# Kernel tuning notes

Hardware: AMD Instinct MI355X
Metric: run time of the kernel (lower is better)

The kernel has to match this reference:

```python
import jax, jax.numpy as jnp
import numpy as np

B, S, D = 2, 2048, 2048
NQ, NKV, H = 16, 8, 256
G = NQ // NKV
SOFT_CAP = 50.0
WINDOW = 1024
MAX_WAVELENGTH = 10000.0


def _rope(x, start_index=0):
    # keras_hub RotaryEmbedding (rotate-half) followed by Gemma's interleave
    # reshape: stack(split(x,2,-1),axis=-1).reshape(shape). Net effect:
    # out[..., 2i] = x1*cos - x2*sin, out[..., 2i+1] = x2*cos + x1*sin.
    b, s, n, h = x.shape
    half = h // 2
    inv_freq = 1.0 / (MAX_WAVELENGTH ** (jnp.arange(0, h, 2, dtype=jnp.float32) / h))
    positions = start_index + jnp.arange(s, dtype=jnp.float32)
    freq = positions[:, None] * inv_freq[None, :]            # (s, h/2)
    cos = jnp.cos(freq)[None, :, None, :].astype(x.dtype)     # (1,s,1,h/2)
    sin = jnp.sin(freq)[None, :, None, :].astype(x.dtype)
    x1, x2 = x[..., :half], x[..., half:]
    r1 = x1 * cos - x2 * sin
    r2 = x2 * cos + x1 * sin
    return jnp.stack([r1, r2], axis=-1).reshape(b, s, n, h)


def setup_inputs() -> dict:
    key = jax.random.key(0)
    ks = jax.random.split(key, 5)
    x = jax.random.normal(ks[0], (B, S, D), dtype=jnp.float32)
    Wq = jax.random.normal(ks[1], (NQ, D, H), dtype=jnp.float32) * 0.02
    Wk = jax.random.normal(ks[2], (NKV, D, H), dtype=jnp.float32) * 0.02
    Wv = jax.random.normal(ks[3], (NKV, D, H), dtype=jnp.float32) * 0.02
    Wo = jax.random.normal(ks[4], (NQ, H, D), dtype=jnp.float32) * 0.02
    attention_mask = jnp.tril(jnp.ones((S, S), dtype=jnp.float32))  # causal
    return {"x": x, "Wq": Wq, "Wk": Wk, "Wv": Wv, "Wo": Wo,
            "attention_mask": attention_mask}


def reference(x, Wq, Wk, Wv, Wo, attention_mask):
    q = _rope(jnp.einsum('btd,ndh->btnh', x, Wq))   # (B,S,NQ,H)
    k = _rope(jnp.einsum('bsd,kdh->bskh', x, Wk))   # (B,S,NKV,H)
    v = jnp.einsum('bsd,kdh->bskh', x, Wv)          # (B,S,NKV,H)

    q = q * jnp.asarray(1.0 / np.sqrt(H), dtype=q.dtype)
    q = q.reshape(B, S, NKV, G, H)
    logits = jnp.einsum('btkgh,bskh->bkgts', q, k).astype(jnp.float32)

    # logit soft-cap
    logits = jnp.tanh(logits / SOFT_CAP) * SOFT_CAP

    # sliding-window band AND causal mask
    ones = jnp.ones((S, S), dtype=jnp.float32)
    sliding = jnp.triu(ones, -(WINDOW - 1)) * jnp.tril(ones, WINDOW - 1)
    mask = sliding * attention_mask                  # (S,S)

    # keras Softmax with mask: masked positions get -1e9 (fp32)
    masked = jnp.where(mask[None, None, None, :, :] > 0, logits,
                       jnp.float32(-1e9))
    probs = jax.nn.softmax(masked, axis=-1).astype(x.dtype)

    av = jnp.einsum('bkgts,bskh->btkgh', probs, v).reshape(B, S, NQ, H)

    # zero rows with no attended tokens (original causal mask)
    na = jnp.all(attention_mask == 0, axis=-1, keepdims=True)[..., None]  # (S,1,1)
    av = jnp.where(na, jnp.zeros_like(av), av)

    return jnp.einsum('btnh,nhd->btd', av, Wo)
```

## Files before the change

### kernel.cpp

```cpp
#include <hip/hip_runtime.h>
#include <stdint.h>

typedef __bf16 bf16_t;
typedef __bf16 bf16x8 __attribute__((ext_vector_type(8)));
typedef __bf16 bf16x4 __attribute__((ext_vector_type(4)));
typedef float f32x4 __attribute__((ext_vector_type(4)));

#define DEV static __device__ __forceinline__

#define SB 2
#define SS 2048
#define SD 2048
#define SNQ 16
#define SNKV 8
#define SH 256
#define SWIN 1024
#define QKVP 8192

DEV void async_ld16(const void* g, void* lds) {
  __builtin_amdgcn_global_load_lds(
      (const __attribute__((address_space(1))) void*)g,
      (__attribute__((address_space(3))) void*)lds, 16, 0, 0);
}

__global__ __launch_bounds__(256) void cvt_kernel(const float* __restrict__ in,
                                                  bf16_t* __restrict__ out) {
  int i = blockIdx.x * 256 + threadIdx.x;
  float4 v = ((const float4*)in)[i];
  bf16x4 o = {(bf16_t)v.x, (bf16_t)v.y, (bf16_t)v.z, (bf16_t)v.w};
  *(bf16x4*)(out + (size_t)i * 4) = o;
}

__global__ __launch_bounds__(256) void wtrans3_kernel(const float* __restrict__ Wq,
                                                      const float* __restrict__ Wk,
                                                      const float* __restrict__ Wv,
                                                      bf16_t* __restrict__ out) {
  __shared__ bf16_t T[64 * 72];
  const int zg = blockIdx.z;
  const float* ip = (zg < 16) ? (Wq + (size_t)zg * SD * SH)
                  : (zg < 24) ? (Wk + (size_t)(zg - 16) * SD * SH)
                              : (Wv + (size_t)(zg - 24) * SD * SH);
  bf16_t* op = out + (size_t)zg * SD * SH;
  const int r0 = blockIdx.y * 64, c0 = blockIdx.x * 64;
  const int tc = threadIdx.x & 15;
  const int tr = threadIdx.x >> 4;
#pragma unroll
  for (int i = 0; i < 4; ++i) {
    const int r = tr + i * 16;
    float4 v = *(const float4*)(ip + (size_t)(r0 + r) * SH + c0 + tc * 4);
    float vv[4] = {v.x, v.y, v.z, v.w};
#pragma unroll
    for (int e = 0; e < 4; ++e) {
      const int row = tc * 4 + e;
      *(bf16_t*)((char*)T + row * 144 + ((r * 2) ^ (((row >> 3) & 7) << 4))) =
          (bf16_t)vv[e];
    }
  }
  __syncthreads();
  const int tc2 = threadIdx.x & 7, tr2 = threadIdx.x >> 3;
#pragma unroll
  for (int i = 0; i < 2; ++i) {
    const int row = tr2 + i * 32;
    bf16x8 v = *(const bf16x8*)((const char*)T + row * 144 +
                                ((tc2 * 16) ^ (((row >> 3) & 7) << 4)));
    *(bf16x8*)(op + (size_t)(c0 + row) * SD + r0 + tc2 * 8) = v;
  }
}

__global__ __launch_bounds__(256) void wtrans_kernel(const float* __restrict__ in,
                                                     bf16_t* __restrict__ out,
                                                     int R, int C) {
  __shared__ bf16_t T[64 * 72];
  const float* ip = in;
  bf16_t* op = out;
  const int r0 = blockIdx.y * 64, c0 = blockIdx.x * 64;
  const int tc = threadIdx.x & 15;
  const int tr = threadIdx.x >> 4;
#pragma unroll
  for (int i = 0; i < 4; ++i) {
    const int r = tr + i * 16;
    float4 v = *(const float4*)(ip + (size_t)(r0 + r) * C + c0 + tc * 4);
    float vv[4] = {v.x, v.y, v.z, v.w};
#pragma unroll
    for (int e = 0; e < 4; ++e) {
      const int row = tc * 4 + e;
      *(bf16_t*)((char*)T + row * 144 + ((r * 2) ^ (((row >> 3) & 7) << 4))) =
          (bf16_t)vv[e];
    }
  }
  __syncthreads();
  const int tc2 = threadIdx.x & 7, tr2 = threadIdx.x >> 3;
#pragma unroll
  for (int i = 0; i < 2; ++i) {
    const int row = tr2 + i * 32;
    bf16x8 v = *(const bf16x8*)((const char*)T + row * 144 +
                                ((tc2 * 16) ^ (((row >> 3) & 7) << 4)));
    *(bf16x8*)(op + (size_t)(c0 + row) * R + r0 + tc2 * 8) = v;
  }
}

template <int BN, int MODE>
__global__ __launch_bounds__(512, 1) void gemm8p(const bf16_t* __restrict__ A,
                                                 const bf16_t* __restrict__ Bt,
                                                 void* __restrict__ Cout,
                                                 bf16_t* __restrict__ kbp,
                                                 bf16_t* __restrict__ vtp,
                                                 int M, int N, int K) {
  constexpr int WM = (BN == 256) ? 2 : 4;
  constexpr int WN = 8 / WM;
  constexpr int MQ = 4 / WM;
  constexpr int BH = BN / 128;
  constexpr int SMEM = 65536 + BH * 32768;
  __shared__ char smem[SMEM];
  bf16_t* AsBase = (bf16_t*)smem;
  bf16_t* BsBase = (bf16_t*)(smem + 65536);

  const int tid = threadIdx.x, lane = tid & 63, wid = tid >> 6;
  const int xcd = blockIdx.x & 7, ii = blockIdx.x >> 3;
  int by, bx;
  if (BN == 256) { by = (xcd & 1) * 8 + (ii >> 3); bx = (xcd >> 1) * 8 + (ii & 7); }
  else           { by = (xcd & 3) * 4 + (ii >> 3); bx = (xcd >> 2) * 8 + (ii & 7); }
  const int row0 = by << 8, col0 = bx * BN;
  const int wr = wid / WN, wc = wid % WN;
  const int lr = lane & 15, hi = lane >> 4;

  const bf16_t* Arow = A + (size_t)row0 * K;
  const bf16_t* Brow = Bt + (size_t)col0 * K;

  auto stageHA = [&](int t, int h) {
#pragma unroll
    for (int i = 0; i < 2; ++i) {
      const int f = tid + (i << 9);
      const int r = (h << 7) + (f >> 3), pc = f & 7;
      async_ld16(Arow + (size_t)r * K + (t << 6) + (pc ^ (r & 7)) * 8,
                 (char*)(AsBase + (t & 1) * (256 * 64)) + (h << 14) + f * 16);
    }
  };
  auto stageHB = [&](int t, int h) {
#pragma unroll
    for (int i = 0; i < 2; ++i) {
      const int f = tid + (i << 9);
      const int r = (h << 7) + (f >> 3), pc = f & 7;
      async_ld16(Brow + (size_t)r * K + (t << 6) + (pc ^ (r & 7)) * 8,
                 (char*)(BsBase + (t & 1) * (BN * 64)) + (h << 14) + f * 16);
    }
  };

  f32x4 acc[4 * MQ][4];
#pragma unroll
  for (int m = 0; m < 4 * MQ; ++m)
#pragma unroll
    for (int n = 0; n < 4; ++n) acc[m][n] = f32x4{0.f, 0.f, 0.f, 0.f};

  const int NT = K >> 6;
  stageHB(0, 0);
  if (BH == 2) stageHB(0, 1);
  stageHA(0, 0); stageHA(0, 1);
  asm volatile("s_waitcnt vmcnt(2)" ::: "memory");
  __builtin_amdgcn_s_barrier();
  __builtin_amdgcn_sched_barrier(0);

  for (int t = 0; t < NT; ++t) {
    const bool pre = (t + 1 < NT);
    const char* Ab = (const char*)(AsBase + (t & 1) * (256 * 64));
    const char* Bb = (const char*)(BsBase + (t & 1) * (BN * 64));
    bf16x8 bfr[4][2];

#pragma unroll
    for (int q = 0; q < 4; ++q) {
      if (q == 0) {
#pragma unroll
        for (int nf = 0; nf < 4; ++nf)
#pragma unroll
          for (int ks = 0; ks < 2; ++ks) {
            const int r = nf * (16 * WN) + wc * 16 + lr;
            bfr[nf][ks] = *(const bf16x8*)(Bb + r * 128 +
                                           ((((ks << 2) + hi) ^ (r & 7)) << 4));
          }
      }
      bf16x8 af[MQ][2];
#pragma unroll
      for (int mq = 0; mq < MQ; ++mq)
#pragma unroll
        for (int ks = 0; ks < 2; ++ks) {
          const int r = q * 64 + mq * (16 * WM) + wr * 16 + lr;
          af[mq][ks] = *(const bf16x8*)(Ab + r * 128 +
                                        ((((ks << 2) + hi) ^ (r & 7)) << 4));
        }
      if (pre) {
        if (BH == 2) {
          if (q == 0) stageHB(t + 1, 0);
          if (q == 1) stageHB(t + 1, 1);
          if (q == 2) stageHA(t + 1, 0);
          if (q == 3) stageHA(t + 1, 1);
        } else {
          if (q == 0) stageHB(t + 1, 0);
          if (q == 1) stageHA(t + 1, 0);
          if (q == 2) stageHA(t + 1, 1);
        }
      }
      __builtin_amdgcn_s_setprio(1);
#pragma unroll
      for (int mq = 0; mq < MQ; ++mq)
#pragma unroll
        for (int nf = 0; nf < 4; ++nf)
#pragma unroll
          for (int ks = 0; ks < 2; ++ks)
            acc[q * MQ + mq][nf] = __builtin_amdgcn_mfma_f32_16x16x32_bf16(
                af[mq][ks], bfr[nf][ks], acc[q * MQ + mq][nf], 0, 0, 0);
      __builtin_amdgcn_s_setprio(0);
      if (q == 1) {
        if (pre) asm volatile("s_waitcnt vmcnt(4)" ::: "memory");
        else     asm volatile("s_waitcnt vmcnt(0)" ::: "memory");
        __builtin_amdgcn_s_barrier();
        __builtin_amdgcn_sched_barrier(0);
      }
      if (q == 3 && pre) {
        asm volatile("s_waitcnt vmcnt(2)" ::: "memory");
        __builtin_amdgcn_s_barrier();
        __builtin_amdgcn_sched_barrier(0);
      }
    }
  }

  if (MODE == 1 && bx >= 16 && bx < 24) {
    const int kv = bx - 16;
#pragma unroll
    for (int mf = 0; mf < 4 * MQ; ++mf) {
      const int r = row0 + (mf / MQ) * 64 + (mf % MQ) * (16 * WM) + wr * 16 + hi * 4;
#pragma unroll
      for (int nfp = 0; nfp < 2; ++nfp) {
        const int h = nfp * 64 + wc * 16 + lr;
        const float inv = __expf((float)h * -0.07195578f);
#pragma unroll
        for (int j = 0; j < 4; ++j) {
          const int rg = r + j;
          const int tpos = rg & (SS - 1), b = rg >> 11;
          const float fr = (float)tpos * inv;
          const float cs = __cosf(fr), sn = __sinf(fr);
          const float x1 = acc[mf][nfp][j], x2 = acc[mf][nfp + 2][j];
          bf16_t* kp = kbp + ((size_t)(b * SNKV + kv) * SS + tpos) * SH + h;
          kp[0] = (bf16_t)(x1 * cs - x2 * sn);
          kp[128] = (bf16_t)(x2 * cs + x1 * sn);
        }
      }
    }
  } else if (MODE == 1 && bx >= 24) {
    bf16_t* T = (bf16_t*)smem;
    __syncthreads();
    const int kv = bx - 24;
#pragma unroll
    for (int mf = 0; mf < 4 * MQ; ++mf) {
      const int tl = (mf / MQ) * 64 + (mf % MQ) * (16 * WM) + wr * 16 + hi * 4;
#pragma unroll
      for (int nf = 0; nf < 4; ++nf) {
        const int h = nf * (16 * WN) + wc * 16 + lr;
        bf16x4 v4 = {(bf16_t)acc[mf][nf][0], (bf16_t)acc[mf][nf][1],
                     (bf16_t)acc[mf][nf][2], (bf16_t)acc[mf][nf][3]};
        *(bf16x4*)((char*)T + h * 512 + ((tl * 2) ^ ((h & 7) << 4))) = v4;
      }
    }
    __syncthreads();
    const int b = row0 >> 11, t0b = row0 & (SS - 1);
    bf16_t* vbase = vtp + (size_t)(b * SNKV + kv) * SH * SS;
#pragma unroll
    for (int it = 0; it < 16; ++it) {
      const int f = tid + (it << 9);
      const int h = f >> 5, sl = f & 31;
      bf16x8 v = *(const bf16x8*)((const char*)T + h * 512 +
                                  ((sl << 4) ^ ((h & 7) << 4)));
      *(bf16x8*)(vbase + (size_t)h * SS + t0b + sl * 8) = v;
    }
  } else {
#pragma unroll
    for (int mf = 0; mf < 4 * MQ; ++mf) {
      const int r = row0 + (mf / MQ) * 64 + (mf % MQ) * (16 * WM) + wr * 16 + hi * 4;
#pragma unroll
      for (int nf = 0; nf < 4; ++nf) {
        const int c = col0 + nf * (16 * WN) + wc * 16 + lr;
#pragma unroll
        for (int j = 0; j < 4; ++j) {
          if (MODE == 2)
            ((float*)Cout)[(size_t)(r + j) * N + c] = acc[mf][nf][j];
          else
            ((bf16_t*)Cout)[(size_t)(r + j) * N + c] = (bf16_t)acc[mf][nf][j];
        }
      }
    }
  }
}

#define QB 128
#define KVB 64
#define PP 72

__global__ __launch_bounds__(512, 2) void attn_kernel(
    const bf16_t* __restrict__ Q,
    const bf16_t* __restrict__ Kt,
    const bf16_t* __restrict__ Vt,
    bf16_t* __restrict__ AV) {
  __shared__ bf16_t Ks[2][KVB * SH];
  __shared__ bf16_t Vs[2][SH * KVB];
  __shared__ bf16_t Ps[QB * PP];

  const int tid = threadIdx.x, lane = tid & 63, wid = tid >> 6;
  const int x = blockIdx.x & 7;
  const int y = blockIdx.x >> 3;
  const int qt = 15 - (y & 15);
  const int head = (x << 1) | ((y >> 4) & 1);
  const int b = y >> 5;
  const int kvh = x;
  const int t0 = qt << 7;
  const int trw = t0 + wid * 16;
  const int lr = lane & 15, hi = lane >> 4;
  const int lk = hi << 3;
  const int lq = hi;

  bf16x8 qf[8];
  {
    const bf16_t* qp = Q + ((size_t)(b * SS + trw + lr)) * QKVP + head * SH + lk;
#pragma unroll
    for (int ks = 0; ks < 8; ++ks) qf[ks] = *(const bf16x8*)(qp + ks * 32);
    const float tpos = (float)(trw + lr);
#pragma unroll
    for (int ks = 0; ks < 4; ++ks) {
      bf16x8 a = qf[ks], b2 = qf[ks + 4];
      bf16x8 ra, rb;
#pragma unroll
      for (int e = 0; e < 8; ++e) {
        float c_ = (float)(ks * 32 + lk + e);
        float inv = __expf(c_ * -0.07195578f);
        float fr = tpos * inv;
        float cs = __cosf(fr), sn = __sinf(fr);
        float x1 = (float)a[e], x2 = (float)b2[e];
        ra[e] = (bf16_t)((x1 * cs - x2 * sn) * 0.0625f);
        rb[e] = (bf16_t)((x2 * cs + x1 * sn) * 0.0625f);
      }
      qf[ks] = ra; qf[ks + 4] = rb;
    }
  }

  f32x4 o[16];
#pragma unroll
  for (int i = 0; i < 16; ++i) o[i] = f32x4{0.f, 0.f, 0.f, 0.f};
  float lsum[4] = {0.f, 0.f, 0.f, 0.f};

  const bf16_t* Kb = Kt + (size_t)(b * SNKV + kvh) * SS * SH;
  const bf16_t* Vb = Vt + (size_t)(b * SNKV + kvh) * SH * SS;

  const int sv0 = (t0 >= SWIN) ? ((t0 >> 6) - 16) : 0;
  const int sv1 = (t0 >> 6) + 1;

  auto stage = [&](int s0, int d) {
#pragma unroll
    for (int it = 0; it < 4; ++it) {
      const int f = tid + (it << 9);
      {
        const int r = f >> 5, pc = f & 31;
        const int sc = pc ^ (r & 7);
        async_ld16(Kb + (size_t)(s0 + r) * SH + sc * 8, (char*)Ks[d] + f * 16);
      }
      {
        const int r = f >> 3, pc = f & 7;
        const int sc = pc ^ (r & 7);
        async_ld16(Vb + (size_t)r * SS + s0 + sc * 8, (char*)Vs[d] + f * 16);
      }
    }
  };

  stage(sv0 << 6, 0);
  __syncthreads();

  int cur = 0;
  for (int sv = sv0; sv <= sv1; ++sv, cur ^= 1) {
    if (sv < sv1) stage((sv + 1) << 6, cur ^ 1);

    const int s0 = sv << 6;
    const bool skip = (s0 > trw + 15) || (s0 + 63 < trw - (SWIN - 1));
    if (!skip) {
      const bf16_t* Kc = Ks[cur];
      const bf16_t* Vc = Vs[cur];
      f32x4 sacc[4];
#pragma unroll
      for (int nt = 0; nt < 4; ++nt) sacc[nt] = f32x4{0.f, 0.f, 0.f, 0.f};
      __builtin_amdgcn_s_setprio(1);
#pragma unroll
      for (int ks = 0; ks < 8; ++ks) {
#pragma unroll
        for (int nt = 0; nt < 4; ++nt) {
          const int R = nt * 16 + lr;
          bf16x8 kf = *(const bf16x8*)((const char*)Kc + R * 512 +
                                       (((ks * 4 + hi) ^ (R & 7)) << 4));
          sacc[nt] = __builtin_amdgcn_mfma_f32_16x16x32_bf16(qf[ks], kf, sacc[nt], 0, 0, 0);
        }
      }
      __builtin_amdgcn_s_setprio(0);

      const bool full = (s0 + 63 <= trw) && (s0 >= trw + 15 - (SWIN - 1));
      if (full) {
#pragma unroll
        for (int nt = 0; nt < 4; ++nt) {
#pragma unroll
          for (int j = 0; j < 4; ++j) {
            float u = sacc[nt][j] * 0.04f;
            float th = 50.f - 100.f * __builtin_amdgcn_rcpf(__expf(u) + 1.f);
            float p = __expf(th);
            lsum[j] += p;
            Ps[(wid * 16 + lq * 4 + j) * PP + nt * 16 + lr] = (bf16_t)p;
          }
        }
      } else {
#pragma unroll
        for (int nt = 0; nt < 4; ++nt) {
          const int s_ = s0 + nt * 16 + lr;
#pragma unroll
          for (int j = 0; j < 4; ++j) {
            const int t_ = trw + lq * 4 + j;
            float u = sacc[nt][j] * 0.04f;
            float th = 50.f - 100.f * __builtin_amdgcn_rcpf(__expf(u) + 1.f);
            const bool valid = (s_ <= t_) && (t_ - s_ < SWIN);
            float p = valid ? __expf(th) : 0.f;
            lsum[j] += p;
            Ps[(wid * 16 + lq * 4 + j) * PP + nt * 16 + lr] = (bf16_t)p;
          }
        }
      }

      __builtin_amdgcn_s_setprio(1);
#pragma unroll
      for (int ks = 0; ks < 2; ++ks) {
        bf16x8 pf = *(const bf16x8*)&Ps[(wid * 16 + lr) * PP + ks * 32 + lk];
#pragma unroll
        for (int nt = 0; nt < 16; ++nt) {
          const int R = nt * 16 + lr;
          bf16x8 vf = *(const bf16x8*)((const char*)Vc + R * 128 +
                                       (((ks * 4 + hi) ^ (R & 7)) << 4));
          o[nt] = __builtin_amdgcn_mfma_f32_16x16x32_bf16(pf, vf, o[nt], 0, 0, 0);
        }
      }
      __builtin_amdgcn_s_setprio(0);
    }

    __syncthreads();
  }

#pragma unroll
  for (int j = 0; j < 4; ++j) {
    float l = lsum[j];
    l += __shfl_xor(l, 1);
    l += __shfl_xor(l, 2);
    l += __shfl_xor(l, 4);
    l += __shfl_xor(l, 8);
    const float inv = 1.f / l;
    const int t_ = trw + lq * 4 + j;
    bf16_t* op = AV + ((size_t)(b * SS + t_)) * (SNQ * SH) + head * SH;
#pragma unroll
    for (int nt = 0; nt < 16; ++nt) op[nt * 16 + lr] = (bf16_t)(o[nt][j] * inv);
  }
}

extern "C" void kernel_launch(void* const* d_in, const int* in_sizes, int n_in,
                              void* d_out, int out_size, void* d_ws, size_t ws_size,
                              hipStream_t stream) {
  const float* x = (const float*)d_in[0];
  const float* Wq = (const float*)d_in[1];
  const float* Wk = (const float*)d_in[2];
  const float* Wv = (const float*)d_in[3];
  const float* Wo = (const float*)d_in[4];
  float* out = (float*)d_out;

  char* ws = (char*)d_ws;
  size_t off = 0;
  auto alloc = [&](size_t elems) {
    bf16_t* p = (bf16_t*)(ws + off);
    off += ((elems * 2 + 255) & ~(size_t)255);
    return p;
  };
  const size_t MS = (size_t)SB * SS;
  bf16_t* xb     = alloc(MS * SD);
  bf16_t* wqkvT  = alloc((size_t)QKVP * SD);
  bf16_t* woT    = alloc((size_t)SD * SNQ * SH);
  bf16_t* qkv    = alloc(MS * QKVP);
  bf16_t* kb     = alloc(MS * SNKV * SH);
  bf16_t* vt     = alloc(MS * SNKV * SH);
  bf16_t* av     = alloc(MS * SNQ * SH);
  (void)ws_size;

  cvt_kernel<<<(MS * SD / 4) / 256, 256, 0, stream>>>(x, xb);
  wtrans3_kernel<<<dim3(SH / 64, SD / 64, 32), 256, 0, stream>>>(Wq, Wk, Wv, wqkvT);
  wtrans_kernel<<<dim3(SD / 64, (SNQ * SH) / 64, 1), 256, 0, stream>>>(Wo, woT, SNQ * SH, SD);

  gemm8p<256, 1><<<512, 512, 0, stream>>>(xb, wqkvT, qkv, kb, vt, 4096, QKVP, 2048);

  attn_kernel<<<512, 512, 0, stream>>>(qkv, kb, vt, av);

  gemm8p<128, 2><<<256, 512, 0, stream>>>(av, woT, out, nullptr, nullptr, 4096, 2048, 4096);
}
```

Measured before the change: 326.4 us.

## Merge prep kernels and restructure GEMM k-loop into 2x2 A/B sub-tiles

Merges the x conversion and the three weight-transpose kernels into one launch, indexing the work by a flattened block id, to cut launch overhead. Restructures the GEMM inner loop so that A fragments for two 64-row quarters are loaded together and B fragments are loaded in halves. The next-tile async loads and the vmcnt/barrier points are re-spread across the four sub-steps. This changes register pressure and the overlap of loads with MFMA work, and the hand-tuned waitcnt values must exactly match the count of outstanding loads.

```diff
diff --git a/kernel.cpp b/kernel.cpp
--- a/kernel.cpp
+++ b/kernel.cpp
@@ -23,57 +23,39 @@
       (__attribute__((address_space(3))) void*)lds, 16, 0, 0);
 }
 
-__global__ __launch_bounds__(256) void cvt_kernel(const float* __restrict__ in,
-                                                  bf16_t* __restrict__ out) {
-  int i = blockIdx.x * 256 + threadIdx.x;
-  float4 v = ((const float4*)in)[i];
-  bf16x4 o = {(bf16_t)v.x, (bf16_t)v.y, (bf16_t)v.z, (bf16_t)v.w};
-  *(bf16x4*)(out + (size_t)i * 4) = o;
-}
-
-__global__ __launch_bounds__(256) void wtrans3_kernel(const float* __restrict__ Wq,
-                                                      const float* __restrict__ Wk,
-                                                      const float* __restrict__ Wv,
-                                                      bf16_t* __restrict__ out) {
+__global__ __launch_bounds__(256) void prep_kernel(
+    const float* __restrict__ x, const float* __restrict__ Wq,
+    const float* __restrict__ Wk, const float* __restrict__ Wv,
+    const float* __restrict__ Wo, bf16_t* __restrict__ xb,
+    bf16_t* __restrict__ wqkvT, bf16_t* __restrict__ woT) {
   __shared__ bf16_t T[64 * 72];
-  const int zg = blockIdx.z;
-  const float* ip = (zg < 16) ? (Wq + (size_t)zg * SD * SH)
-                  : (zg < 24) ? (Wk + (size_t)(zg - 16) * SD * SH)
-                              : (Wv + (size_t)(zg - 24) * SD * SH);
-  bf16_t* op = out + (size_t)zg * SD * SH;
-  const int r0 = blockIdx.y * 64, c0 = blockIdx.x * 64;
-  const int tc = threadIdx.x & 15;
-  const int tr = threadIdx.x >> 4;
-#pragma unroll
-  for (int i = 0; i < 4; ++i) {
-    const int r = tr + i * 16;
-    float4 v = *(const float4*)(ip + (size_t)(r0 + r) * SH + c0 + tc * 4);
-    float vv[4] = {v.x, v.y, v.z, v.w};
-#pragma unroll
-    for (int e = 0; e < 4; ++e) {
-      const int row = tc * 4 + e;
-      *(bf16_t*)((char*)T + row * 144 + ((r * 2) ^ (((row >> 3) & 7) << 4))) =
-          (bf16_t)vv[e];
-    }
-  }
-  __syncthreads();
-  const int tc2 = threadIdx.x & 7, tr2 = threadIdx.x >> 3;
-#pragma unroll
-  for (int i = 0; i < 2; ++i) {
-    const int row = tr2 + i * 32;
-    bf16x8 v = *(const bf16x8*)((const char*)T + row * 144 +
-                                ((tc2 * 16) ^ (((row >> 3) & 7) << 4)));
-    *(bf16x8*)(op + (size_t)(c0 + row) * SD + r0 + tc2 * 8) = v;
-  }
-}
-
-__global__ __launch_bounds__(256) void wtrans_kernel(const float* __restrict__ in,
-                                                     bf16_t* __restrict__ out,
-                                                     int R, int C) {
-  __shared__ bf16_t T[64 * 72];
-  const float* ip = in;
-  bf16_t* op = out;
-  const int r0 = blockIdx.y * 64, c0 = blockIdx.x * 64;
+  int bid = blockIdx.x;
+  if (bid < 8192) {
+    const int i = bid * 256 + threadIdx.x;
+    float4 v = ((const float4*)x)[i];
+    bf16x4 o = {(bf16_t)v.x, (bf16_t)v.y, (bf16_t)v.z, (bf16_t)v.w};
+    *(bf16x4*)(xb + (size_t)i * 4) = o;
+    return;
+  }
+  bid -= 8192;
+  const float* ip;
+  bf16_t* op;
+  int R, C, r0, c0;
+  if (bid < 4096) {
+    const int zg = bid >> 7, rest = bid & 127;
+    r0 = (rest >> 2) * 64;
+    c0 = (rest & 3) * 64;
+    ip = (zg < 16) ? (Wq + (size_t)zg * SD * SH)
+       : (zg < 24) ? (Wk + (size_t)(zg - 16) * SD * SH)
+                   : (Wv + (size_t)(zg - 24) * SD * SH);
+    op = wqkvT + (size_t)zg * SD * SH;
+    R = SD; C = SH;
+  } else {
+    bid -= 4096;
+    r0 = (bid >> 5) * 64;
+    c0 = (bid & 31) * 64;
+    ip = Wo; op = woT; R = SNQ * SH; C = SD;
+  }
   const int tc = threadIdx.x & 15;
   const int tr = threadIdx.x >> 4;
 #pragma unroll
@@ -153,10 +135,13 @@
     for (int n = 0; n < 4; ++n) acc[m][n] = f32x4{0.f, 0.f, 0.f, 0.f};
 
   const int NT = K >> 6;
-  stageHB(0, 0);
-  if (BH == 2) stageHB(0, 1);
-  stageHA(0, 0); stageHA(0, 1);
-  asm volatile("s_waitcnt vmcnt(2)" ::: "memory");
+  if (BH == 2) {
+    stageHB(0, 0); stageHA(0, 0); stageHB(0, 1); stageHA(0, 1);
+    asm volatile("s_waitcnt vmcnt(4)" ::: "memory");
+  } else {
+    stageHB(0, 0); stageHA(0, 0); stageHA(0, 1);
+    asm volatile("s_waitcnt vmcnt(2)" ::: "memory");
+  }
   __builtin_amdgcn_s_barrier();
   __builtin_amdgcn_sched_barrier(0);
 
@@ -164,61 +149,70 @@
     const bool pre = (t + 1 < NT);
     const char* Ab = (const char*)(AsBase + (t & 1) * (256 * 64));
     const char* Bb = (const char*)(BsBase + (t & 1) * (BN * 64));
-    bf16x8 bfr[4][2];
-
-#pragma unroll
-    for (int q = 0; q < 4; ++q) {
-      if (q == 0) {
-#pragma unroll
-        for (int nf = 0; nf < 4; ++nf)
+
+#pragma unroll
+    for (int pa = 0; pa < 2; ++pa) {
+      bf16x8 af[2][MQ][2];
+#pragma unroll
+      for (int qq = 0; qq < 2; ++qq)
+#pragma unroll
+        for (int mq = 0; mq < MQ; ++mq)
 #pragma unroll
           for (int ks = 0; ks < 2; ++ks) {
-            const int r = nf * (16 * WN) + wc * 16 + lr;
-            bfr[nf][ks] = *(const bf16x8*)(Bb + r * 128 +
+            const int r = (pa * 2 + qq) * 64 + mq * (16 * WM) + wr * 16 + lr;
+            af[qq][mq][ks] = *(const bf16x8*)(Ab + r * 128 +
+                                              ((((ks << 2) + hi) ^ (r & 7)) << 4));
+          }
+#pragma unroll
+      for (int pb = 0; pb < 2; ++pb) {
+        bf16x8 bfr[2][2];
+#pragma unroll
+        for (int bn = 0; bn < 2; ++bn)
+#pragma unroll
+          for (int ks = 0; ks < 2; ++ks) {
+            const int r = (pb * 2 + bn) * (16 * WN) + wc * 16 + lr;
+            bfr[bn][ks] = *(const bf16x8*)(Bb + r * 128 +
                                            ((((ks << 2) + hi) ^ (r & 7)) << 4));
           }
-      }
-      bf16x8 af[MQ][2];
-#pragma unroll
-      for (int mq = 0; mq < MQ; ++mq)
-#pragma unroll
-        for (int ks = 0; ks < 2; ++ks) {
-          const int r = q * 64 + mq * (16 * WM) + wr * 16 + lr;
-          af[mq][ks] = *(const bf16x8*)(Ab + r * 128 +
-                                        ((((ks << 2) + hi) ^ (r & 7)) << 4));
-        }
-      if (pre) {
-        if (BH == 2) {
-          if (q == 0) stageHB(t + 1, 0);
-          if (q == 1) stageHB(t + 1, 1);
-          if (q == 2) stageHA(t + 1, 0);
-          if (q == 3) stageHA(t + 1, 1);
-        } else {
-          if (q == 0) stageHB(t + 1, 0);
-          if (q == 1) stageHA(t + 1, 0);
-          if (q == 2) stageHA(t + 1, 1);
-        }
-      }
-      __builtin_amdgcn_s_setprio(1);
-#pragma unroll
-      for (int mq = 0; mq < MQ; ++mq)
-#pragma unroll
-        for (int nf = 0; nf < 4; ++nf)
-#pragma unroll
-          for (int ks = 0; ks < 2; ++ks)
-            acc[q * MQ + mq][nf] = __builtin_amdgcn_mfma_f32_16x16x32_bf16(
-                af[mq][ks], bfr[nf][ks], acc[q * MQ + mq][nf], 0, 0, 0);
-      __builtin_amdgcn_s_setprio(0);
-      if (q == 1) {
-        if (pre) asm volatile("s_waitcnt vmcnt(4)" ::: "memory");
-        else     asm volatile("s_waitcnt vmcnt(0)" ::: "memory");
-        __builtin_amdgcn_s_barrier();
-        __builtin_amdgcn_sched_barrier(0);
-      }
-      if (q == 3 && pre) {
-        asm volatile("s_waitcnt vmcnt(2)" ::: "memory");
-        __builtin_amdgcn_s_barrier();
-        __builtin_amdgcn_sched_barrier(0);
+        if (pre) {
+          if (pa == 0 && pb == 0) stageHB(t + 1, 0);
+          if (pa == 0 && pb == 1) stageHA(t + 1, 0);
+          if (pa == 1 && pb == 0 && BH == 2) stageHB(t + 1, 1);
+          if (pa == 1 && pb == 1) stageHA(t + 1, 1);
+        }
+        __builtin_amdgcn_s_setprio(1);
+#pragma unroll
+        for (int qq = 0; qq < 2; ++qq)
+#pragma unroll
+          for (int mq = 0; mq < MQ; ++mq)
+#pragma unroll
+            for (int bn = 0; bn < 2; ++bn)
+#pragma unroll
+              for (int ks = 0; ks < 2; ++ks)
+                acc[(pa * 2 + qq) * MQ + mq][pb * 2 + bn] =
+                    __builtin_amdgcn_mfma_f32_16x16x32_bf16(
+                        af[qq][mq][ks], bfr[bn][ks],
+                        acc[(pa * 2 + qq) * MQ + mq][pb * 2 + bn], 0, 0, 0);
+        __builtin_amdgcn_s_setprio(0);
+
+        if (pa == 0 && pb == 0 && BH == 2) {
+          if (pre) asm volatile("s_waitcnt vmcnt(4)" ::: "memory");
+          else     asm volatile("s_waitcnt vmcnt(2)" ::: "memory");
+          __builtin_amdgcn_s_barrier();
+          __builtin_amdgcn_sched_barrier(0);
+        }
+        if (pa == 0 && pb == 1) {
+          if (pre) asm volatile("s_waitcnt vmcnt(4)" ::: "memory");
+          else     asm volatile("s_waitcnt vmcnt(0)" ::: "memory");
+          __builtin_amdgcn_s_barrier();
+          __builtin_amdgcn_sched_barrier(0);
+        }
+        if (pa == 1 && pb == 1 && pre) {
+          if (BH == 2) asm volatile("s_waitcnt vmcnt(4)" ::: "memory");
+          else         asm volatile("s_waitcnt vmcnt(2)" ::: "memory");
+          __builtin_amdgcn_s_barrier();
+          __builtin_amdgcn_sched_barrier(0);
+        }
       }
     }
   }
@@ -486,9 +480,7 @@
   bf16_t* av     = alloc(MS * SNQ * SH);
   (void)ws_size;
 
-  cvt_kernel<<<(MS * SD / 4) / 256, 256, 0, stream>>>(x, xb);
-  wtrans3_kernel<<<dim3(SH / 64, SD / 64, 32), 256, 0, stream>>>(Wq, Wk, Wv, wqkvT);
-  wtrans_kernel<<<dim3(SD / 64, (SNQ * SH) / 64, 1), 256, 0, stream>>>(Wo, woT, SNQ * SH, SD);
+  prep_kernel<<<14336, 256, 0, stream>>>(x, Wq, Wk, Wv, Wo, xb, wqkvT, woT);
 
   gemm8p<256, 1><<<512, 512, 0, stream>>>(xb, wqkvT, qkv, kb, vt, 4096, QKVP, 2048);
 
```

After: 325.5 us. Within noise of the previous version (-0.3%).
